# Kernel tuning notes

Hardware: AMD Instinct MI355X
Metric: run time of the kernel (lower is better)

Reference implementation:

```python
import jax, jax.numpy as jnp
import numpy as np

HEADS = 16
MAX_DIST = 1024

def setup_inputs() -> dict:
    key = jax.random.key(0)
    k1, k2, k3, k4 = jax.random.split(key, 4)
    b, n, dim = 2, 2048, 1024
    x = jax.random.normal(k1, (b, n, dim), dtype=jnp.float32)
    W_qkv = jax.random.normal(k2, (3 * dim, dim), dtype=jnp.float32) * (dim ** -0.5)
    W_out = jax.random.normal(k3, (dim, dim), dtype=jnp.float32) * (dim ** -0.5)
    b_out = jnp.zeros((dim,), dtype=jnp.float32)
    rel_emb = jax.random.normal(k4, (2 * MAX_DIST + 1, HEADS), dtype=jnp.float32) * 0.02
    return {"x": x, "W_qkv": W_qkv, "W_out": W_out, "b_out": b_out, "rel_emb": rel_emb}

def reference(x, W_qkv, W_out, b_out, rel_emb):
    b, n, dim = x.shape
    h = HEADS
    d = dim // h
    scale = d ** -0.5
    qkv = jnp.einsum('bnd,ed->bne', x, W_qkv)  # [b, n, 3*dim]
    q, k, v = jnp.split(qkv, 3, axis=-1)
    def to_heads(t):
        return t.reshape(b, n, h, d).transpose(0, 2, 1, 3)  # b h n d
    q, k, v = to_heads(q), to_heads(k), to_heads(v)
    # relative position bias: [1, h, n, n]
    dist = jnp.arange(n)[None, :] - jnp.arange(n)[:, None]
    idx = jnp.clip(dist, -MAX_DIST, MAX_DIST) + MAX_DIST  # [n, n]
    rel_bias = rel_emb[idx].transpose(2, 0, 1)[None]  # [1, h, n, n]
    scores = jnp.einsum('bhqd,bhkd->bhqk', q, k) * scale + rel_bias
    attn = jax.nn.softmax(scores, axis=-1)
    out = jnp.einsum('bhqk,bhkd->bhqd', attn, v)
    out = out.transpose(0, 2, 1, 3).reshape(b, n, dim)
    return jnp.einsum('bnd,ed->bne', out, W_out) + b_out
```

## Files before the change

### kernel.cpp

```cpp
#include <hip/hip_runtime.h>
#include <hip/hip_bf16.h>

typedef __attribute__((ext_vector_type(8))) short short8;
typedef __attribute__((ext_vector_type(4))) float f32x4;
typedef __attribute__((ext_vector_type(16))) float f32x16;
typedef float f32x4u __attribute__((ext_vector_type(4), aligned(4)));
typedef __attribute__((ext_vector_type(4))) unsigned short u16x4;
typedef __attribute__((ext_vector_type(2))) unsigned int u32x2;
typedef __attribute__((ext_vector_type(4))) unsigned int u32x4;
typedef __hip_bfloat16 bf16;

#define SCALE_Q 0.18033688f

#define GLD_LDS16(g, l) __builtin_amdgcn_global_load_lds(                      \
    (const __attribute__((address_space(1))) void*)(g),                        \
    (__attribute__((address_space(3))) void*)(l), 16, 0, 0)

static __device__ __forceinline__ f32x4 mfma16(short8 a, short8 b, f32x4 c) {
  return __builtin_amdgcn_mfma_f32_16x16x32_bf16(a, b, c, 0, 0, 0);
}
static __device__ __forceinline__ f32x16 mfma32(short8 a, short8 b, f32x16 c) {
  return __builtin_amdgcn_mfma_f32_32x32x16_bf16(a, b, c, 0, 0, 0);
}

static __device__ __forceinline__ unsigned cvtpk(float lo, float hi) {
  unsigned r;
  asm("v_cvt_pk_bf16_f32 %0, %1, %2" : "=v"(r) : "v"(lo), "v"(hi));
  return r;
}

static __device__ __forceinline__ float fexp2(float x) {
  float r;
  asm("v_exp_f32 %0, %1" : "=v"(r) : "v"(x));
  return r;
}

static __device__ __forceinline__ float bf2f(unsigned short u) {
  return __builtin_bit_cast(float, (unsigned)u << 16);
}

#define PLSWAP(a, b) asm("v_permlane32_swap_b32 %0, %1" : "+v"(a), "+v"(b))

__global__ __launch_bounds__(256) void k_pre(
    const float* __restrict__ x, const float* __restrict__ Wqkv,
    const float* __restrict__ Wout, const float* __restrict__ rel,
    bf16* __restrict__ xb, bf16* __restrict__ wqb, bf16* __restrict__ wob,
    float* __restrict__ relpf) {
  int bid = blockIdx.x;
  if (bid < 4096) {
    const float* in;
    bf16* out;
    long i;
    if (bid < 2048) {
      in = x; out = xb; i = (long)bid * 256 + threadIdx.x;
    } else if (bid < 3584) {
      in = Wqkv; out = wqb; i = (long)(bid - 2048) * 256 + threadIdx.x;
    } else {
      in = Wout; out = wob; i = (long)(bid - 3584) * 256 + threadIdx.x;
    }
    f32x4 v0 = *(const f32x4*)(in + i * 8);
    f32x4 v1 = *(const f32x4*)(in + i * 8 + 4);
    u32x4 o;
    o[0] = cvtpk(v0[0], v0[1]);
    o[1] = cvtpk(v0[2], v0[3]);
    o[2] = cvtpk(v1[0], v1[1]);
    o[3] = cvtpk(v1[2], v1[3]);
    *(u32x4*)((unsigned short*)out + i * 8) = o;
  } else {
    int base = (bid - 4096) * 1024 + threadIdx.x;
#pragma unroll
    for (int k = 0; k < 4; ++k) {
      int i = base + k * 256;
      int h = i >> 12, ii = i & 4095;
      int dd = ii - 2047;
      dd = dd < -1024 ? -1024 : (dd > 1024 ? 1024 : dd);
      relpf[i] = rel[(size_t)(dd + 1024) * 16 + h] * 1.44269504f - 16.0f;
    }
  }
}

__global__ __launch_bounds__(256, 3) void k_gemm(
    const bf16* __restrict__ A, const bf16* __restrict__ B,
    int M, int N, int K, int epi,
    bf16* __restrict__ Qb, bf16* __restrict__ Kb, bf16* __restrict__ Vt,
    float* __restrict__ Out, const float* __restrict__ bias) {
  __shared__ bf16 lA[3][4096];
  __shared__ bf16 lB[3][4096];
  const int tid = threadIdx.x, w = tid >> 6, l = tid & 63;
  const int m0 = blockIdx.x * 128, n0 = blockIdx.y * 128;
  const int wrow = (w >> 1) * 64, wcol = (w & 1) * 64;
  const int fr = l & 15, fq = l >> 4;
  f32x4 acc[4][4] = {};
  const int c0 = w * 64 + l, c1 = c0 + 256;
  const bf16* Ag0 = A + (size_t)(m0 + (c0 >> 2)) * K + (c0 & 3) * 8;
  const bf16* Ag1 = A + (size_t)(m0 + (c1 >> 2)) * K + (c1 & 3) * 8;
  const bf16* Bg0 = B + (size_t)(n0 + (c0 >> 2)) * K + (c0 & 3) * 8;
  const bf16* Bg1 = B + (size_t)(n0 + (c1 >> 2)) * K + (c1 & 3) * 8;
  bf16* lA0 = &lA[0][w * 512];
  bf16* lA1 = &lA[0][2048 + w * 512];
  bf16* lB0 = &lB[0][w * 512];
  bf16* lB1 = &lB[0][2048 + w * 512];

#define GSTAGE(T, BI)                                                          \
  do {                                                                         \
    const int ko_ = (T) * 32;                                                  \
    GLD_LDS16(Ag0 + ko_, lA0 + (BI) * 4096);                                   \
    GLD_LDS16(Ag1 + ko_, lA1 + (BI) * 4096);                                   \
    GLD_LDS16(Bg0 + ko_, lB0 + (BI) * 4096);                                   \
    GLD_LDS16(Bg1 + ko_, lB1 + (BI) * 4096);                                   \
  } while (0)

  const int nk = K >> 5;
  GSTAGE(0, 0);
  __builtin_amdgcn_sched_barrier(0);
  GSTAGE(1, 1);
  __builtin_amdgcn_sched_barrier(0);

  int bc_ = 0, bs_ = 2;
  for (int t = 0; t < nk; ++t) {
    asm volatile("s_waitcnt vmcnt(4)" ::: "memory");
    __builtin_amdgcn_s_barrier();
    __builtin_amdgcn_sched_barrier(0);
    int tt = (t + 2 < nk) ? t + 2 : nk - 1;
    GSTAGE(tt, bs_);
    __builtin_amdgcn_sched_barrier(0);
    const bf16* pA = &lA[bc_][0];
    const bf16* pB = &lB[bc_][0];
    short8 af[4], bfv[4];
#pragma unroll
    for (int mi = 0; mi < 4; ++mi)
      af[mi] = *(const short8*)&pA[(wrow + mi * 16 + fr) * 32 + fq * 8];
#pragma unroll
    for (int ni = 0; ni < 4; ++ni)
      bfv[ni] = *(const short8*)&pB[(wcol + ni * 16 + fr) * 32 + fq * 8];
    __builtin_amdgcn_s_setprio(1);
#pragma unroll
    for (int mi = 0; mi < 4; ++mi)
#pragma unroll
      for (int ni = 0; ni < 4; ++ni)
        acc[mi][ni] = mfma16(bfv[ni], af[mi], acc[mi][ni]);
    __builtin_amdgcn_s_setprio(0);
    bc_ = (bc_ == 2) ? 0 : bc_ + 1;
    bs_ = (bs_ == 2) ? 0 : bs_ + 1;
  }
#undef GSTAGE

  if (epi == 0) {
#pragma unroll
    for (int mi = 0; mi < 4; ++mi)
#pragma unroll
      for (int ni = 0; ni < 4; ++ni) {
        int t = m0 + wrow + mi * 16 + fr;
        int e4 = n0 + wcol + ni * 16 + fq * 4;
        int sect = e4 >> 10, eh = (e4 >> 6) & 15, dh = e4 & 63;
        int b = t >> 11, tt = t & 2047;
        f32x4 a = acc[mi][ni];
        if (sect < 2) {
          size_t idx = (((size_t)b * 16 + eh) * 2048 + tt) * 64 + dh;
          float sc = (sect == 0) ? SCALE_Q : 1.f;
          u32x2 ov;
          ov[0] = cvtpk(a[0] * sc, a[1] * sc);
          ov[1] = cvtpk(a[2] * sc, a[3] * sc);
          bf16* dst = (sect == 0) ? Qb : Kb;
          *(u32x2*)(dst + idx) = ov;
        } else {
          size_t vb = ((size_t)((b << 4) + eh) * 64 + dh) * 2048 + tt;
          unsigned p0 = cvtpk(a[0], a[1]);
          unsigned p1 = cvtpk(a[2], a[3]);
          unsigned short* vp = (unsigned short*)Vt;
          vp[vb] = (unsigned short)p0;
          vp[vb + 2048] = (unsigned short)(p0 >> 16);
          vp[vb + 4096] = (unsigned short)p1;
          vp[vb + 6144] = (unsigned short)(p1 >> 16);
        }
      }
  } else {
#pragma unroll
    for (int mi = 0; mi < 4; ++mi)
#pragma unroll
      for (int ni = 0; ni < 4; ++ni) {
        int t = m0 + wrow + mi * 16 + fr;
        int e4 = n0 + wcol + ni * 16 + fq * 4;
        f32x4 bv = *(const f32x4*)(bias + e4);
        f32x4 a = acc[mi][ni];
        f32x4 o = {a[0] + bv[0], a[1] + bv[1], a[2] + bv[2], a[3] + bv[3]};
        *(f32x4*)(Out + (size_t)t * N + e4) = o;
      }
  }
}

__global__ __launch_bounds__(256, 2) void k_attn(
    const bf16* __restrict__ Qb, const bf16* __restrict__ Kb,
    const bf16* __restrict__ Vt, const float* __restrict__ relpf,
    bf16* __restrict__ Op, float2* __restrict__ ML) {
  __shared__ bf16 lK[2][4096];
  __shared__ bf16 lV[2][4096];

  const int id = blockIdx.x;
  const int xcd = id & 7, j = id >> 3;
  const int bh = xcd * 4 + (j >> 4);
  const int rem = j & 15, qt = rem >> 1, sp = rem & 1;
  const int h = bh & 15;
  const int tid = threadIdx.x, w = tid >> 6, l = tid & 63;
  const int r32 = l & 31, hl = l >> 5, rs7 = r32 & 7;
  const int q0 = qt * 256 + w * 64;

  const bf16* Kbh = Kb + (size_t)bh * 2048 * 64;
  const bf16* Vbh = Vt + (size_t)bh * 64 * 2048;
  const int r0 = tid >> 3, c0s = ((tid & 7) ^ (r0 & 7)) * 8;
  const int r1 = (tid + 256) >> 3, c1s = ((tid & 7) ^ (r1 & 7)) * 8;
  const bf16* Ks0 = Kbh + (size_t)r0 * 64 + c0s;
  const bf16* Ks1 = Kbh + (size_t)r1 * 64 + c1s;
  const bf16* Vs0 = Vbh + (size_t)r0 * 2048 + c0s;
  const bf16* Vs1 = Vbh + (size_t)r1 * 2048 + c1s;

#define STAGE(KT, BI)                                                          \
  do {                                                                         \
    GLD_LDS16(Ks0 + (size_t)(KT) * 64, &lK[BI][tid * 8]);                      \
    GLD_LDS16(Ks1 + (size_t)(KT) * 64, &lK[BI][(tid + 256) * 8]);              \
    GLD_LDS16(Vs0 + (KT), &lV[BI][tid * 8]);                                   \
    GLD_LDS16(Vs1 + (KT), &lV[BI][(tid + 256) * 8]);                           \
  } while (0)

  const bf16* Qp = Qb + ((size_t)bh * 2048 + q0 + r32) * 64;
  short8 qf0[4], qf1[4];
#pragma unroll
  for (int ks = 0; ks < 4; ++ks) {
    qf0[ks] = *(const short8*)(Qp + ks * 16 + hl * 8);
    qf1[ks] = *(const short8*)(Qp + 32 * 64 + ks * 16 + hl * 8);
  }

  const float* bp0 = relpf + h * 4096 + (2047 + 4 * hl - q0 - r32);
  const float* bp1 = bp0 - 32;

  float ll0 = 0.f, ll1 = 0.f;
  f32x16 oa0 = {}, ob0 = {}, oa1 = {}, ob1 = {};

  const int kvb = sp * 1024;
  STAGE(kvb, 0);
  __builtin_amdgcn_sched_barrier(0);

  int cur = 0;
  for (int t = 0; t < 16; ++t) {
    const int kt = kvb + t * 64;
    asm volatile("s_waitcnt vmcnt(0)" ::: "memory");
    __builtin_amdgcn_s_barrier();
    __builtin_amdgcn_sched_barrier(0);
    f32x16 sa[2], sb[2];
#pragma unroll
    for (int kb = 0; kb < 2; ++kb)
#pragma unroll
      for (int g = 0; g < 4; ++g) {
        f32x4u va = *(const f32x4u*)(bp0 + kt + kb * 32 + 8 * g);
        f32x4u vb = *(const f32x4u*)(bp1 + kt + kb * 32 + 8 * g);
#pragma unroll
        for (int e = 0; e < 4; ++e) {
          sa[kb][g * 4 + e] = va[e];
          sb[kb][g * 4 + e] = vb[e];
        }
      }
    __builtin_amdgcn_sched_barrier(0);
    if (t < 15) STAGE(kt + 64, cur ^ 1);
    __builtin_amdgcn_sched_barrier(0);
    const bf16* lKc = &lK[cur][0];
    const bf16* lVc = &lV[cur][0];
    __builtin_amdgcn_s_setprio(1);
#pragma unroll
    for (int kb = 0; kb < 2; ++kb)
#pragma unroll
      for (int ks = 0; ks < 4; ++ks) {
        short8 kf = *(const short8*)&lKc[(kb * 32 + r32) * 64 +
                                         (((2 * ks + hl) ^ rs7) * 8)];
        sa[kb] = mfma32(kf, qf0[ks], sa[kb]);
        sb[kb] = mfma32(kf, qf1[ks], sb[kb]);
      }
    __builtin_amdgcn_s_setprio(0);
    float ra[4] = {0.f, 0.f, 0.f, 0.f}, rb[4] = {0.f, 0.f, 0.f, 0.f};
#pragma unroll
    for (int kb = 0; kb < 2; ++kb)
#pragma unroll
      for (int reg = 0; reg < 16; ++reg) {
        sa[kb][reg] = fexp2(sa[kb][reg]);
        ra[reg & 3] += sa[kb][reg];
        sb[kb][reg] = fexp2(sb[kb][reg]);
        rb[reg & 3] += sb[kb][reg];
      }
    ll0 += (ra[0] + ra[1]) + (ra[2] + ra[3]);
    ll1 += (rb[0] + rb[1]) + (rb[2] + rb[3]);
#pragma unroll
    for (int kb = 0; kb < 2; ++kb) {
#pragma unroll
      for (int kh = 0; kh < 2; ++kh) {
        const int e = kh * 8;
        const int ks = kb * 2 + kh;
        const int cc = ((2 * ks + hl) ^ rs7) * 8;
        unsigned a0 = cvtpk(sa[kb][e + 0], sa[kb][e + 1]);
        unsigned a1 = cvtpk(sa[kb][e + 2], sa[kb][e + 3]);
        unsigned b0 = cvtpk(sa[kb][e + 4], sa[kb][e + 5]);
        unsigned b1 = cvtpk(sa[kb][e + 6], sa[kb][e + 7]);
        PLSWAP(a0, b0);
        PLSWAP(a1, b1);
        u32x4 pw0 = {a0, a1, b0, b1};
        short8 pf0 = __builtin_bit_cast(short8, pw0);
        unsigned c0 = cvtpk(sb[kb][e + 0], sb[kb][e + 1]);
        unsigned c1 = cvtpk(sb[kb][e + 2], sb[kb][e + 3]);
        unsigned d0 = cvtpk(sb[kb][e + 4], sb[kb][e + 5]);
        unsigned d1 = cvtpk(sb[kb][e + 6], sb[kb][e + 7]);
        PLSWAP(c0, d0);
        PLSWAP(c1, d1);
        u32x4 pw1 = {c0, c1, d0, d1};
        short8 pf1 = __builtin_bit_cast(short8, pw1);
        short8 v0 = *(const short8*)&lVc[r32 * 64 + cc];
        short8 v1 = *(const short8*)&lVc[(32 + r32) * 64 + cc];
        __builtin_amdgcn_s_setprio(1);
        oa0 = mfma32(v0, pf0, oa0);
        ob0 = mfma32(v1, pf0, ob0);
        oa1 = mfma32(v0, pf1, oa1);
        ob1 = mfma32(v1, pf1, ob1);
        __builtin_amdgcn_s_setprio(0);
      }
    }
    cur ^= 1;
  }
#undef STAGE

  float l0t = ll0 + __shfl_xor(ll0, 32);
  float l1t = ll1 + __shfl_xor(ll1, 32);
  float rin0 = 1.f / l0t, rin1 = 1.f / l1t;
  bf16* ao0 = Op + (((size_t)sp * 32 + bh) * 2048 + q0 + r32) * 64 + hl * 4;
  bf16* ao1 = ao0 + 32 * 64;
#pragma unroll
  for (int rg = 0; rg < 4; ++rg) {
    u32x2 ov;
    ov[0] = cvtpk(oa0[4 * rg + 0] * rin0, oa0[4 * rg + 1] * rin0);
    ov[1] = cvtpk(oa0[4 * rg + 2] * rin0, oa0[4 * rg + 3] * rin0);
    *(u32x2*)(ao0 + rg * 8) = ov;
    ov[0] = cvtpk(ob0[4 * rg + 0] * rin0, ob0[4 * rg + 1] * rin0);
    ov[1] = cvtpk(ob0[4 * rg + 2] * rin0, ob0[4 * rg + 3] * rin0);
    *(u32x2*)(ao0 + 32 + rg * 8) = ov;
    ov[0] = cvtpk(oa1[4 * rg + 0] * rin1, oa1[4 * rg + 1] * rin1);
    ov[1] = cvtpk(oa1[4 * rg + 2] * rin1, oa1[4 * rg + 3] * rin1);
    *(u32x2*)(ao1 + rg * 8) = ov;
    ov[0] = cvtpk(ob1[4 * rg + 0] * rin1, ob1[4 * rg + 1] * rin1);
    ov[1] = cvtpk(ob1[4 * rg + 2] * rin1, ob1[4 * rg + 3] * rin1);
    *(u32x2*)(ao1 + 32 + rg * 8) = ov;
  }
  if (hl == 0) {
    size_t li = ((size_t)sp * 32 + bh) * 2048;
    float2 v0;
    v0.x = -16.f;
    v0.y = l0t;
    ML[li + q0 + r32] = v0;
    float2 v1;
    v1.x = -16.f;
    v1.y = l1t;
    ML[li + q0 + 32 + r32] = v1;
  }
}

__global__ __launch_bounds__(256) void k_comb(const bf16* __restrict__ Op,
                                              const float2* __restrict__ ML,
                                              bf16* __restrict__ AO) {
  int idx = blockIdx.x * 256 + threadIdx.x;
  int d8 = idx & 7, q = (idx >> 3) & 2047, bh = idx >> 14;
  int h = bh & 15, b = bh >> 4;
  size_t mli = (size_t)bh * 2048 + q;
  float2 ml0 = ML[mli];
  float2 ml1 = ML[65536 + mli];
  float m = fmaxf(ml0.x, ml1.x);
  float w0 = ml0.y * fexp2(ml0.x - m);
  float w1 = ml1.y * fexp2(ml1.x - m);
  float rin = 1.f / (w0 + w1);
  w0 *= rin;
  w1 *= rin;
  size_t off = ((size_t)bh * 2048 + q) * 64 + d8 * 8;
  short8 o0 = *(const short8*)(Op + off);
  short8 o1 = *(const short8*)(Op + 4194304 + off);
  u32x4 ov;
#pragma unroll
  for (int p = 0; p < 4; ++p) {
    float fa = w0 * bf2f((unsigned short)o0[2 * p]) +
               w1 * bf2f((unsigned short)o1[2 * p]);
    float fb = w0 * bf2f((unsigned short)o0[2 * p + 1]) +
               w1 * bf2f((unsigned short)o1[2 * p + 1]);
    ov[p] = cvtpk(fa, fb);
  }
  *(u32x4*)(AO + ((size_t)(b * 2048 + q)) * 1024 + h * 64 + d8 * 8) = ov;
}

extern "C" void kernel_launch(void* const* d_in, const int* in_sizes, int n_in,
                              void* d_out, int out_size, void* d_ws,
                              size_t ws_size, hipStream_t stream) {
  const float* x = (const float*)d_in[0];
  const float* Wqkv = (const float*)d_in[1];
  const float* Wout = (const float*)d_in[2];
  const float* bout = (const float*)d_in[3];
  const float* rel = (const float*)d_in[4];
  float* out = (float*)d_out;

  char* p = (char*)d_ws;
  bf16* xb  = (bf16*)(p);
  bf16* wqb = (bf16*)(p + (8ull << 20));
  bf16* wob = (bf16*)(p + (16ull << 20));
  bf16* Qb  = (bf16*)(p + (18ull << 20));
  bf16* Kb  = (bf16*)(p + (26ull << 20));
  bf16* Vtr = (bf16*)(p + (34ull << 20));
  bf16* aob = (bf16*)(p + (42ull << 20));
  float* relpf = (float*)(p + (50ull << 20));
  float2* ML = (float2*)(p + (51ull << 20));
  bf16* Opart = (bf16*)(p);

  k_pre<<<4160, 256, 0, stream>>>(x, Wqkv, Wout, rel, xb, wqb, wob, relpf);
  k_gemm<<<dim3(32, 24), 256, 0, stream>>>(xb, wqb, 4096, 3072, 1024, 0,
                                           Qb, Kb, Vtr, nullptr, nullptr);
  k_attn<<<512, 256, 0, stream>>>(Qb, Kb, Vtr, relpf, Opart, ML);
  k_comb<<<2048, 256, 0, stream>>>(Opart, ML, aob);
  k_gemm<<<dim3(32, 8), 256, 0, stream>>>(aob, wob, 4096, 1024, 1024, 1,
                                          nullptr, nullptr, nullptr, out, bout);
}
```

Before: 124.1 us.

## Move split-KV combine inside attention block and drop combine kernel

Each attention block now handles 128 query rows. Its four waves are split into two query halves times two KV halves, with separate double-buffered K/V LDS tiles per KV half. At the end, the second KV half writes its partial output and row sums to LDS, and the first half merges them, normalizes, and writes the head-interleaved output directly. This removes the separate k_comb launch and the round trip of partial outputs through global memory. The cost is twice the LDS per block and each K/V tile being shared by only two waves instead of four, which raises load traffic per query.

```diff
diff --git a/kernel.cpp b/kernel.cpp
--- a/kernel.cpp
+++ b/kernel.cpp
@@ -192,34 +192,40 @@
 __global__ __launch_bounds__(256, 2) void k_attn(
     const bf16* __restrict__ Qb, const bf16* __restrict__ Kb,
     const bf16* __restrict__ Vt, const float* __restrict__ relpf,
-    bf16* __restrict__ Op, float2* __restrict__ ML) {
-  __shared__ bf16 lK[2][4096];
-  __shared__ bf16 lV[2][4096];
+    bf16* __restrict__ AO) {
+  __shared__ bf16 lK[2][2][4096];
+  __shared__ bf16 lV[2][2][4096];
 
   const int id = blockIdx.x;
   const int xcd = id & 7, j = id >> 3;
-  const int bh = xcd * 4 + (j >> 4);
-  const int rem = j & 15, qt = rem >> 1, sp = rem & 1;
-  const int h = bh & 15;
+  const int bh = xcd * 4 + (j >> 4), qt = j & 15;
+  const int h = bh & 15, b = bh >> 4;
   const int tid = threadIdx.x, w = tid >> 6, l = tid & 63;
   const int r32 = l & 31, hl = l >> 5, rs7 = r32 & 7;
-  const int q0 = qt * 256 + w * 64;
+  const int qh = w & 1, kvh = w >> 1;
+  const int kvb = kvh * 1024;
+  const int q0 = qt * 128 + qh * 64;
 
   const bf16* Kbh = Kb + (size_t)bh * 2048 * 64;
   const bf16* Vbh = Vt + (size_t)bh * 64 * 2048;
-  const int r0 = tid >> 3, c0s = ((tid & 7) ^ (r0 & 7)) * 8;
-  const int r1 = (tid + 256) >> 3, c1s = ((tid & 7) ^ (r1 & 7)) * 8;
-  const bf16* Ks0 = Kbh + (size_t)r0 * 64 + c0s;
-  const bf16* Ks1 = Kbh + (size_t)r1 * 64 + c1s;
-  const bf16* Vs0 = Vbh + (size_t)r0 * 2048 + c0s;
-  const bf16* Vs1 = Vbh + (size_t)r1 * 2048 + c1s;
+  const int pl = tid & 127;
+  const bf16* Ksp[4];
+  const bf16* Vsp[4];
+#pragma unroll
+  for (int s = 0; s < 4; ++s) {
+    int ck = pl + 128 * s;
+    int kr = ck >> 3, kc = (ck & 7) ^ (kr & 7);
+    Ksp[s] = Kbh + (size_t)kr * 64 + kc * 8;
+    Vsp[s] = Vbh + (size_t)kr * 2048 + kc * 8;
+  }
 
 #define STAGE(KT, BI)                                                          \
   do {                                                                         \
-    GLD_LDS16(Ks0 + (size_t)(KT) * 64, &lK[BI][tid * 8]);                      \
-    GLD_LDS16(Ks1 + (size_t)(KT) * 64, &lK[BI][(tid + 256) * 8]);              \
-    GLD_LDS16(Vs0 + (KT), &lV[BI][tid * 8]);                                   \
-    GLD_LDS16(Vs1 + (KT), &lV[BI][(tid + 256) * 8]);                           \
+    _Pragma("unroll") for (int s_ = 0; s_ < 4; ++s_) {                         \
+      int ck_ = pl + 128 * s_;                                                 \
+      GLD_LDS16(Ksp[s_] + (size_t)(KT) * 64, &lK[kvh][BI][ck_ * 8]);           \
+      GLD_LDS16(Vsp[s_] + (KT), &lV[kvh][BI][ck_ * 8]);                        \
+    }                                                                          \
   } while (0)
 
   const bf16* Qp = Qb + ((size_t)bh * 2048 + q0 + r32) * 64;
@@ -236,7 +242,6 @@
   float ll0 = 0.f, ll1 = 0.f;
   f32x16 oa0 = {}, ob0 = {}, oa1 = {}, ob1 = {};
 
-  const int kvb = sp * 1024;
   STAGE(kvb, 0);
   __builtin_amdgcn_sched_barrier(0);
 
@@ -262,8 +267,8 @@
     __builtin_amdgcn_sched_barrier(0);
     if (t < 15) STAGE(kt + 64, cur ^ 1);
     __builtin_amdgcn_sched_barrier(0);
-    const bf16* lKc = &lK[cur][0];
-    const bf16* lVc = &lV[cur][0];
+    const bf16* lKc = &lK[kvh][cur][0];
+    const bf16* lVc = &lV[kvh][cur][0];
     __builtin_amdgcn_s_setprio(1);
 #pragma unroll
     for (int kb = 0; kb < 2; ++kb)
@@ -326,66 +331,63 @@
 
   float l0t = ll0 + __shfl_xor(ll0, 32);
   float l1t = ll1 + __shfl_xor(ll1, 32);
-  float rin0 = 1.f / l0t, rin1 = 1.f / l1t;
-  bf16* ao0 = Op + (((size_t)sp * 32 + bh) * 2048 + q0 + r32) * 64 + hl * 4;
-  bf16* ao1 = ao0 + 32 * 64;
-#pragma unroll
-  for (int rg = 0; rg < 4; ++rg) {
-    u32x2 ov;
-    ov[0] = cvtpk(oa0[4 * rg + 0] * rin0, oa0[4 * rg + 1] * rin0);
-    ov[1] = cvtpk(oa0[4 * rg + 2] * rin0, oa0[4 * rg + 3] * rin0);
-    *(u32x2*)(ao0 + rg * 8) = ov;
-    ov[0] = cvtpk(ob0[4 * rg + 0] * rin0, ob0[4 * rg + 1] * rin0);
-    ov[1] = cvtpk(ob0[4 * rg + 2] * rin0, ob0[4 * rg + 3] * rin0);
-    *(u32x2*)(ao0 + 32 + rg * 8) = ov;
-    ov[0] = cvtpk(oa1[4 * rg + 0] * rin1, oa1[4 * rg + 1] * rin1);
-    ov[1] = cvtpk(oa1[4 * rg + 2] * rin1, oa1[4 * rg + 3] * rin1);
-    *(u32x2*)(ao1 + rg * 8) = ov;
-    ov[0] = cvtpk(ob1[4 * rg + 0] * rin1, ob1[4 * rg + 1] * rin1);
-    ov[1] = cvtpk(ob1[4 * rg + 2] * rin1, ob1[4 * rg + 3] * rin1);
-    *(u32x2*)(ao1 + 32 + rg * 8) = ov;
-  }
-  if (hl == 0) {
-    size_t li = ((size_t)sp * 32 + bh) * 2048;
-    float2 v0;
-    v0.x = -16.f;
-    v0.y = l0t;
-    ML[li + q0 + r32] = v0;
-    float2 v1;
-    v1.x = -16.f;
-    v1.y = l1t;
-    ML[li + q0 + 32 + r32] = v1;
-  }
-}
-
-__global__ __launch_bounds__(256) void k_comb(const bf16* __restrict__ Op,
-                                              const float2* __restrict__ ML,
-                                              bf16* __restrict__ AO) {
-  int idx = blockIdx.x * 256 + threadIdx.x;
-  int d8 = idx & 7, q = (idx >> 3) & 2047, bh = idx >> 14;
-  int h = bh & 15, b = bh >> 4;
-  size_t mli = (size_t)bh * 2048 + q;
-  float2 ml0 = ML[mli];
-  float2 ml1 = ML[65536 + mli];
-  float m = fmaxf(ml0.x, ml1.x);
-  float w0 = ml0.y * fexp2(ml0.x - m);
-  float w1 = ml1.y * fexp2(ml1.x - m);
-  float rin = 1.f / (w0 + w1);
-  w0 *= rin;
-  w1 *= rin;
-  size_t off = ((size_t)bh * 2048 + q) * 64 + d8 * 8;
-  short8 o0 = *(const short8*)(Op + off);
-  short8 o1 = *(const short8*)(Op + 4194304 + off);
-  u32x4 ov;
-#pragma unroll
-  for (int p = 0; p < 4; ++p) {
-    float fa = w0 * bf2f((unsigned short)o0[2 * p]) +
-               w1 * bf2f((unsigned short)o1[2 * p]);
-    float fb = w0 * bf2f((unsigned short)o0[2 * p + 1]) +
-               w1 * bf2f((unsigned short)o1[2 * p + 1]);
-    ov[p] = cvtpk(fa, fb);
-  }
-  *(u32x4*)(AO + ((size_t)(b * 2048 + q)) * 1024 + h * 64 + d8 * 8) = ov;
+  __syncthreads();
+  char* pbase = (qh == 0) ? (char*)&lK[0][0][0] : (char*)&lV[0][0][0];
+  float* lf = (float*)(pbase + 64 * 136);
+  unsigned* pw = (unsigned*)(pbase + l * 136);
+  if (kvh == 1) {
+#pragma unroll
+    for (int k = 0; k < 8; ++k) {
+      pw[k] = cvtpk(oa0[2 * k], oa0[2 * k + 1]);
+      pw[8 + k] = cvtpk(ob0[2 * k], ob0[2 * k + 1]);
+      pw[16 + k] = cvtpk(oa1[2 * k], oa1[2 * k + 1]);
+      pw[24 + k] = cvtpk(ob1[2 * k], ob1[2 * k + 1]);
+    }
+    if (hl == 0) {
+      lf[r32] = l0t;
+      lf[32 + r32] = l1t;
+    }
+  }
+  __syncthreads();
+  if (kvh == 0) {
+    float ls0 = l0t + lf[r32];
+    float ls1 = l1t + lf[32 + r32];
+#pragma unroll
+    for (int k = 0; k < 8; ++k) {
+      unsigned u;
+      u = pw[k];
+      oa0[2 * k] += bf2f((unsigned short)u);
+      oa0[2 * k + 1] += bf2f((unsigned short)(u >> 16));
+      u = pw[8 + k];
+      ob0[2 * k] += bf2f((unsigned short)u);
+      ob0[2 * k + 1] += bf2f((unsigned short)(u >> 16));
+      u = pw[16 + k];
+      oa1[2 * k] += bf2f((unsigned short)u);
+      oa1[2 * k + 1] += bf2f((unsigned short)(u >> 16));
+      u = pw[24 + k];
+      ob1[2 * k] += bf2f((unsigned short)u);
+      ob1[2 * k + 1] += bf2f((unsigned short)(u >> 16));
+    }
+    float rin0 = 1.f / ls0, rin1 = 1.f / ls1;
+    bf16* aor = AO + ((size_t)(b * 2048 + q0 + r32)) * 1024 + h * 64 + hl * 4;
+    bf16* ao1 = aor + (size_t)32 * 1024;
+#pragma unroll
+    for (int rg = 0; rg < 4; ++rg) {
+      u32x2 ov;
+      ov[0] = cvtpk(oa0[4 * rg + 0] * rin0, oa0[4 * rg + 1] * rin0);
+      ov[1] = cvtpk(oa0[4 * rg + 2] * rin0, oa0[4 * rg + 3] * rin0);
+      *(u32x2*)(aor + rg * 8) = ov;
+      ov[0] = cvtpk(ob0[4 * rg + 0] * rin0, ob0[4 * rg + 1] * rin0);
+      ov[1] = cvtpk(ob0[4 * rg + 2] * rin0, ob0[4 * rg + 3] * rin0);
+      *(u32x2*)(aor + 32 + rg * 8) = ov;
+      ov[0] = cvtpk(oa1[4 * rg + 0] * rin1, oa1[4 * rg + 1] * rin1);
+      ov[1] = cvtpk(oa1[4 * rg + 2] * rin1, oa1[4 * rg + 3] * rin1);
+      *(u32x2*)(ao1 + rg * 8) = ov;
+      ov[0] = cvtpk(ob1[4 * rg + 0] * rin1, ob1[4 * rg + 1] * rin1);
+      ov[1] = cvtpk(ob1[4 * rg + 2] * rin1, ob1[4 * rg + 3] * rin1);
+      *(u32x2*)(ao1 + 32 + rg * 8) = ov;
+    }
+  }
 }
 
 extern "C" void kernel_launch(void* const* d_in, const int* in_sizes, int n_in,
@@ -401,20 +403,17 @@
   char* p = (char*)d_ws;
   bf16* xb  = (bf16*)(p);
   bf16* wqb = (bf16*)(p + (8ull << 20));
-  bf16* wob = (bf16*)(p + (16ull << 20));
-  bf16* Qb  = (bf16*)(p + (18ull << 20));
-  bf16* Kb  = (bf16*)(p + (26ull << 20));
-  bf16* Vtr = (bf16*)(p + (34ull << 20));
-  bf16* aob = (bf16*)(p + (42ull << 20));
-  float* relpf = (float*)(p + (50ull << 20));
-  float2* ML = (float2*)(p + (51ull << 20));
-  bf16* Opart = (bf16*)(p);
+  bf16* wob = (bf16*)(p + (14ull << 20));
+  bf16* Qb  = (bf16*)(p + (16ull << 20));
+  bf16* Kb  = (bf16*)(p + (24ull << 20));
+  bf16* Vtr = (bf16*)(p + (32ull << 20));
+  bf16* aob = (bf16*)(p + (40ull << 20));
+  float* relpf = (float*)(p + (48ull << 20));
 
   k_pre<<<4160, 256, 0, stream>>>(x, Wqkv, Wout, rel, xb, wqb, wob, relpf);
   k_gemm<<<dim3(32, 24), 256, 0, stream>>>(xb, wqb, 4096, 3072, 1024, 0,
                                            Qb, Kb, Vtr, nullptr, nullptr);
-  k_attn<<<512, 256, 0, stream>>>(Qb, Kb, Vtr, relpf, Opart, ML);
-  k_comb<<<2048, 256, 0, stream>>>(Opart, ML, aob);
+  k_attn<<<512, 256, 0, stream>>>(Qb, Kb, Vtr, relpf, aob);
   k_gemm<<<dim3(32, 8), 256, 0, stream>>>(aob, wob, 4096, 1024, 1024, 1,
                                           nullptr, nullptr, nullptr, out, bout);
 }
```

Measured after the change: 119.0 us. 4.2% less time.
